# Kernel tuning notes

Hardware: AMD Instinct MI355X
Metric: run time of the kernel (lower is better)

## Reference

```python
import jax, jax.numpy as jnp
import numpy as np

B, T, H = 2, 1024, 4096
HK, HV, DK, DV = 8, 32, 64, 64
VPK = HV // HK            # value heads per key head = 4
KEY_DIM = HK * DK         # 512
VAL_DIM = HV * DV         # 2048
CONV_DIM = 2 * KEY_DIM + VAL_DIM  # 3072
KSZ = 4
EPS = 1e-5
L2_EPS = 1e-6


def _l2norm(x):
    return x * jax.lax.rsqrt(jnp.sum(x * x, axis=-1, keepdims=True) + L2_EPS)


def setup_inputs() -> dict:
    key = jax.random.key(0)
    ks = jax.random.split(key, 8)
    s = 0.02
    return {
        "hidden_states": jax.random.normal(ks[0], (B, T, H), jnp.float32),
        "W_qkvz": jax.random.normal(ks[1], (H, 2 * KEY_DIM + 2 * VAL_DIM), jnp.float32) * s,
        "W_ba": jax.random.normal(ks[2], (H, 2 * HV), jnp.float32) * s,
        "conv_w": jax.random.normal(ks[3], (CONV_DIM, KSZ), jnp.float32) * 0.1,
        "dt_bias": jnp.ones((HV,), jnp.float32),
        "A_log": jnp.log(jax.random.uniform(ks[4], (HV,), jnp.float32, 1.0, 16.0)),
        "norm_w": jnp.ones((DV,), jnp.float32),
        "W_out": jax.random.normal(ks[5], (VAL_DIM, H), jnp.float32) * s,
    }


def _forward(hidden_states, W_qkvz, W_ba, conv_w, dt_bias, A_log, norm_w, W_out):
    # --- projections ---
    qkvz = hidden_states @ W_qkvz                       # [B,T,5120]
    ba = hidden_states @ W_ba                           # [B,T,64]
    # fix_query_key_value_ordering: per key head [q(Dk), k(Dk), v(vpk*Dv), z(vpk*Dv)]
    qkvz = qkvz.reshape(B, T, HK, 2 * DK + 2 * VPK * DV)
    q = qkvz[..., :DK]                                  # [B,T,HK,DK]
    k = qkvz[..., DK:2 * DK]
    v = qkvz[..., 2 * DK:2 * DK + VPK * DV].reshape(B, T, HV, DV)
    z = qkvz[..., 2 * DK + VPK * DV:].reshape(B, T, HV, DV)
    ba = ba.reshape(B, T, HK, 2 * VPK)
    b = ba[..., :VPK].reshape(B, T, HV)
    a = ba[..., VPK:].reshape(B, T, HV)

    # --- causal depthwise conv over concatenated qkv, then silu ---
    mixed = jnp.concatenate(
        [q.reshape(B, T, KEY_DIM), k.reshape(B, T, KEY_DIM), v.reshape(B, T, VAL_DIM)], axis=-1)
    padded = jnp.pad(mixed, ((0, 0), (KSZ - 1, 0), (0, 0)))
    conv = sum(padded[:, j:j + T, :] * conv_w[:, j] for j in range(KSZ))
    conv = jax.nn.silu(conv)
    q = conv[..., :KEY_DIM].reshape(B, T, HK, DK)
    k = conv[..., KEY_DIM:2 * KEY_DIM].reshape(B, T, HK, DK)
    v = conv[..., 2 * KEY_DIM:].reshape(B, T, HV, DV)

    # --- fused GDN gating: g = -exp(A_log)*softplus(a+dt_bias), beta = sigmoid(b) ---
    g = -jnp.exp(A_log) * jax.nn.softplus(a + dt_bias)  # [B,T,HV]
    beta = jax.nn.sigmoid(b)                            # [B,T,HV]

    # --- q/k l2 norm + scale, broadcast key heads to value heads ---
    q = _l2norm(q) * (DK ** -0.5)
    k = _l2norm(k)
    q = jnp.repeat(q, VPK, axis=2)                      # [B,T,HV,DK]
    k = jnp.repeat(k, VPK, axis=2)

    # --- gated delta-rule recurrence over time ---
    def step(S, inp):
        qt, kt, vt, gt, bt = inp                        # qt/kt [B,HV,DK], vt [B,HV,DV]
        S = S * jnp.exp(gt)[..., None, None]            # decay
        pred = jnp.einsum('bhk,bhkv->bhv', kt, S)
        delta = (vt - pred) * bt[..., None]
        S = S + jnp.einsum('bhk,bhv->bhkv', kt, delta)
        o = jnp.einsum('bhk,bhkv->bhv', qt, S)
        return S, o

    xs = (q.transpose(1, 0, 2, 3), k.transpose(1, 0, 2, 3), v.transpose(1, 0, 2, 3),
          g.transpose(1, 0, 2), beta.transpose(1, 0, 2))
    S0 = jnp.zeros((B, HV, DK, DV), q.dtype)
    _, o = jax.lax.scan(step, S0, xs)                   # [T,B,HV,DV]
    o = o.transpose(1, 0, 2, 3)                         # [B,T,HV,DV]

    # --- gated RMSNorm (norm before gate) + out projection ---
    o_n = o * jax.lax.rsqrt(jnp.mean(o * o, axis=-1, keepdims=True) + EPS) * norm_w
    o_n = o_n * jax.nn.silu(z)
    return o_n.reshape(B, T, VAL_DIM) @ W_out           # [B,T,H]


def reference(hidden_states, W_qkvz, W_ba, conv_w, dt_bias, A_log, norm_w, W_out):
    return _forward(hidden_states, W_qkvz, W_ba, conv_w, dt_bias, A_log, norm_w, W_out)
```

## Files before the change

kernel.cpp:

```cpp
#include <hip/hip_runtime.h>
#include <hip/hip_bf16.h>
#include <cstdint>
#include <cstddef>


typedef __attribute__((ext_vector_type(8))) short short8;
typedef __attribute__((ext_vector_type(4))) float f32x4;

__device__ __forceinline__ short f2bf(float f) {
  union { float f; unsigned u; } x; x.f = f;
  unsigned r = x.u + 0x7fffu + ((x.u >> 16) & 1u);
  return (short)(r >> 16);
}

__device__ __forceinline__ void gl_lds16(const short* g, short* l) {
  __builtin_amdgcn_global_load_lds(
      (const __attribute__((address_space(1))) void*)g,
      (__attribute__((address_space(3))) void*)l, 16, 0, 0);
}

__global__ __launch_bounds__(256) void to_bf16_kernel(const float* __restrict__ x,
                                                      short* __restrict__ y) {
  int i = blockIdx.x * 256 + threadIdx.x;
  float4 v = ((const float4*)x)[i];
  ushort4 r;
  r.x = (unsigned short)f2bf(v.x);
  r.y = (unsigned short)f2bf(v.y);
  r.z = (unsigned short)f2bf(v.z);
  r.w = (unsigned short)f2bf(v.w);
  ((ushort4*)y)[i] = r;
}

__global__ __launch_bounds__(256) void transpose_w1(const float* __restrict__ Wq,
                                                    const float* __restrict__ Wba,
                                                    short* __restrict__ Wt) {
  __shared__ float tile[32][33];
  int n0 = blockIdx.x * 32;
  int k0 = blockIdx.y * 32;
  int t = threadIdx.x;
  int r = t >> 5;
  int c = t & 31;
#pragma unroll
  for (int i = 0; i < 4; ++i) {
    int kl = r + i * 8;
    int n = n0 + c;
    float v = 0.f;
    if (n < 5120) v = Wq[(size_t)(k0 + kl) * 5120 + n];
    else if (n < 5184) v = Wba[(size_t)(k0 + kl) * 64 + (n - 5120)];
    tile[kl][c] = v;
  }
  __syncthreads();
#pragma unroll
  for (int i = 0; i < 4; ++i) {
    int nl = r + i * 8;
    int kl = c;
    Wt[(size_t)(n0 + nl) * 4096 + k0 + kl] = f2bf(tile[kl][nl]);
  }
}

__global__ __launch_bounds__(256) void transpose_w2(const float* __restrict__ W,
                                                    short* __restrict__ Wt) {
  __shared__ float tile[32][33];
  int n0 = blockIdx.x * 32;
  int k0 = blockIdx.y * 32;
  int t = threadIdx.x;
  int r = t >> 5;
  int c = t & 31;
#pragma unroll
  for (int i = 0; i < 4; ++i) {
    int kl = r + i * 8;
    tile[kl][c] = W[(size_t)(k0 + kl) * 4096 + n0 + c];
  }
  __syncthreads();
#pragma unroll
  for (int i = 0; i < 4; ++i) {
    int nl = r + i * 8;
    int kl = c;
    Wt[(size_t)(n0 + nl) * 2048 + k0 + kl] = f2bf(tile[kl][nl]);
  }
}

template <bool GUARD_N>
__global__ __launch_bounds__(256) void gemm128(const short* __restrict__ A,
                                               const short* __restrict__ Bt,
                                               float* __restrict__ C,
                                               int M, int N, int K) {
  __shared__ __align__(16) short As[128 * 32];
  __shared__ __align__(16) short Bs[128 * 32];
  const int tid = threadIdx.x;
  const int wave = tid >> 6;
  const int lane = tid & 63;
  const int m0 = blockIdx.x * 128;
  const int n0 = blockIdx.y * 128;
  const int wm = (wave >> 1) << 6;
  const int wn = (wave & 1) << 6;

  const int srow = (wave << 4) + (lane >> 2);
  const int scol = (lane & 3) << 3;
  const short* Ag = A + (size_t)(m0 + srow) * K + scol;
  const short* Bg = Bt + (size_t)(n0 + srow) * K + scol;
  const size_t rstep = (size_t)64 * K;

  const int fr = lane & 15;
  const int kq = (lane >> 4) << 3;

  f32x4 acc[4][4];
#pragma unroll
  for (int i = 0; i < 4; ++i)
#pragma unroll
    for (int j = 0; j < 4; ++j) acc[i][j] = (f32x4){0.f, 0.f, 0.f, 0.f};

  for (int k0 = 0; k0 < K; k0 += 32) {
    __syncthreads();
    gl_lds16(Ag + k0,         &As[wave * 512]);
    gl_lds16(Ag + rstep + k0, &As[2048 + wave * 512]);
    gl_lds16(Bg + k0,         &Bs[wave * 512]);
    gl_lds16(Bg + rstep + k0, &Bs[2048 + wave * 512]);
    __syncthreads();
    short8 af[4], bf[4];
#pragma unroll
    for (int i = 0; i < 4; ++i) {
      af[i] = *(const short8*)&As[(wm + i * 16 + fr) * 32 + kq];
      bf[i] = *(const short8*)&Bs[(wn + i * 16 + fr) * 32 + kq];
    }
#pragma unroll
    for (int mt = 0; mt < 4; ++mt)
#pragma unroll
      for (int nt = 0; nt < 4; ++nt)
        acc[mt][nt] = __builtin_amdgcn_mfma_f32_16x16x32_bf16(af[mt], bf[nt], acc[mt][nt], 0, 0, 0);
  }

  const int rbase = (lane >> 4) << 2;
#pragma unroll
  for (int mt = 0; mt < 4; ++mt) {
#pragma unroll
    for (int nt = 0; nt < 4; ++nt) {
      int ncol = n0 + wn + nt * 16 + fr;
      if (GUARD_N && ncol >= N) continue;
      int mrow = m0 + wm + mt * 16 + rbase;
#pragma unroll
      for (int r = 0; r < 4; ++r)
        C[(size_t)(mrow + r) * N + ncol] = acc[mt][nt][r];
    }
  }
}

__global__ __launch_bounds__(256) void conv_kernel(const float* __restrict__ qkvz,
                                                   const float* __restrict__ conv_w,
                                                   float* __restrict__ mix) {
  __shared__ float sq[1024];
  __shared__ float scale[16];
  int bt = blockIdx.x;
  int t = bt & 1023;
  int tid = threadIdx.x;
  for (int c = tid; c < 3072; c += 256) {
    int col;
    if (c < 512) {
      col = (c >> 6) * 640 + (c & 63);
    } else if (c < 1024) {
      int c2 = c - 512;
      col = (c2 >> 6) * 640 + 64 + (c2 & 63);
    } else {
      int c3 = c - 1024;
      int hv = c3 >> 6;
      col = (hv >> 2) * 640 + 128 + (hv & 3) * 64 + (c3 & 63);
    }
    float acc = 0.f;
#pragma unroll
    for (int j = 0; j < 4; ++j) {
      int tt = t - 3 + j;
      if (tt >= 0) acc += qkvz[(size_t)(bt - 3 + j) * 5184 + col] * conv_w[c * 4 + j];
    }
    float sv = acc / (1.f + __expf(-acc));
    if (c < 1024)
      sq[c] = sv;
    else
      mix[(size_t)bt * 3072 + c] = sv;
  }
  __syncthreads();
  int g = tid >> 4, l = tid & 15;
  float p = 0.f;
#pragma unroll
  for (int i = 0; i < 4; ++i) {
    float v = sq[g * 64 + l * 4 + i];
    p += v * v;
  }
  p += __shfl_xor(p, 1);
  p += __shfl_xor(p, 2);
  p += __shfl_xor(p, 4);
  p += __shfl_xor(p, 8);
  if (l == 0) scale[g] = rsqrtf(p + 1e-6f);
  __syncthreads();
  for (int c = tid; c < 1024; c += 256) {
    float s = scale[c >> 6] * ((c < 512) ? 0.125f : 1.f);
    mix[(size_t)bt * 3072 + c] = sq[c] * s;
  }
}

__global__ __launch_bounds__(256) void gate_kernel(const float* __restrict__ qkvz,
                                                   const float* __restrict__ dt_bias,
                                                   const float* __restrict__ A_log,
                                                   float* __restrict__ gb,
                                                   float* __restrict__ beta) {
  int i = blockIdx.x * 256 + threadIdx.x;
  int hv = i & 31;
  int bt = i >> 5;
  int hk = hv >> 2, vp = hv & 3;
  const float* row = qkvz + (size_t)bt * 5184 + 5120 + hk * 8;
  float bv = row[vp];
  float av = row[4 + vp];
  float x = av + dt_bias[hv];
  float sp = (x > 20.f) ? x : log1pf(expf(x));
  gb[i] = -expf(A_log[hv]) * sp;
  beta[i] = 1.f / (1.f + expf(-bv));
}

__global__ __launch_bounds__(256) void precompute_kernel(
    const float* __restrict__ mix, const float* __restrict__ gbuf,
    const float* __restrict__ betab, float* __restrict__ Wbuf,
    float* __restrict__ Pbuf, float* __restrict__ Rbuf, float* __restrict__ cbuf) {
  __shared__ float Kt[64][68];
  __shared__ float Vb[64][68];
  __shared__ float AM[64][68];
  __shared__ float Mm[64][68];
  __shared__ float Tb[16][17];
  __shared__ float cs[64], bb[64];

  const int u = blockIdx.x;
  const int chunk = u & 15, hv = (u >> 4) & 31, b = u >> 9;
  const int hk = hv >> 2;
  const int t0g = b * 1024 + chunk * 64;
  const int tid = threadIdx.x;
  const int tr = tid >> 2, q4 = tid & 3;

  {
    const float* mrow = mix + (size_t)(t0g + tr) * 3072;
#pragma unroll
    for (int e = 0; e < 4; ++e) {
      int c0 = q4 * 16 + e * 4;
      float4 kv = *(const float4*)(mrow + 512 + hk * 64 + c0);
      Kt[c0 + 0][tr] = kv.x; Kt[c0 + 1][tr] = kv.y;
      Kt[c0 + 2][tr] = kv.z; Kt[c0 + 3][tr] = kv.w;
      *(float4*)&Vb[tr][c0] = *(const float4*)(mrow + 1024 + hv * 64 + c0);
    }
  }
  if (tid < 64) {
    cs[tid] = gbuf[(size_t)(t0g + tid) * 32 + hv];
    bb[tid] = betab[(size_t)(t0g + tid) * 32 + hv];
  }
  __syncthreads();
  for (int off = 1; off < 64; off <<= 1) {
    float v = 0.f;
    if (tid < 64 && tid >= off) v = cs[tid - off];
    __syncthreads();
    if (tid < 64) cs[tid] += v;
    __syncthreads();
  }
  if (tid < 64) cbuf[(size_t)u * 64 + tid] = cs[tid];

  {
    float acc[16];
#pragma unroll
    for (int i = 0; i < 16; ++i) acc[i] = 0.f;
    for (int d = 0; d < 64; ++d) {
      float kv = Kt[d][tr];
#pragma unroll
      for (int e = 0; e < 4; ++e) {
        float4 ks = *(const float4*)&Kt[d][q4 * 16 + e * 4];
        acc[e * 4 + 0] += kv * ks.x; acc[e * 4 + 1] += kv * ks.y;
        acc[e * 4 + 2] += kv * ks.z; acc[e * 4 + 3] += kv * ks.w;
      }
    }
    float bt_ = bb[tr], ct_ = cs[tr];
#pragma unroll
    for (int j = 0; j < 16; ++j) {
      int s = q4 * 16 + j;
      AM[tr][s] = (s < tr) ? bt_ * acc[j] * __expf(ct_ - cs[s]) : 0.f;
    }
  }
  __syncthreads();

  for (int i = tid; i < 64 * 68; i += 256) (&Mm[0][0])[i] = 0.f;
  __syncthreads();
  if (tid < 64) {
    int blk = tid >> 4, j = tid & 15, base = blk * 16;
    Mm[base][base + j] = (j == 0) ? 1.f : 0.f;
    for (int r = 1; r < 16; ++r) {
      float sum = 0.f;
      for (int s = 0; s < r; ++s) sum += AM[base + r][base + s] * Mm[base + s][base + j];
      Mm[base + r][base + j] = ((r == j) ? 1.f : 0.f) - sum;
    }
  }
  __syncthreads();
  for (int d = 1; d < 4; ++d) {
    for (int j = 0; j + d < 4; ++j) {
      int i = j + d;
      int r = tid >> 4, c = tid & 15;
      float tsum = 0.f;
      for (int kb = j; kb < i; ++kb)
        for (int uu = 0; uu < 16; ++uu)
          tsum += AM[i * 16 + r][kb * 16 + uu] * Mm[kb * 16 + uu][j * 16 + c];
      Tb[r][c] = tsum;
      __syncthreads();
      float msum = 0.f;
      for (int uu = 0; uu < 16; ++uu)
        msum += Mm[i * 16 + r][i * 16 + uu] * Tb[uu][c];
      __syncthreads();
      Mm[i * 16 + r][j * 16 + c] = -msum;
      __syncthreads();
    }
  }

  {
    const float* mrow = mix + (size_t)(t0g + tr) * 3072 + hk * 64;
#pragma unroll
    for (int e = 0; e < 4; ++e) {
      int c0 = q4 * 16 + e * 4;
      float4 qv = *(const float4*)(mrow + c0);
      AM[c0 + 0][tr] = qv.x; AM[c0 + 1][tr] = qv.y;
      AM[c0 + 2][tr] = qv.z; AM[c0 + 3][tr] = qv.w;
    }
  }
  __syncthreads();

  {
    float acc[16];
#pragma unroll
    for (int i = 0; i < 16; ++i) acc[i] = 0.f;
    for (int d = 0; d < 64; ++d) {
      float qv = AM[d][tr];
#pragma unroll
      for (int e = 0; e < 4; ++e) {
        float4 ks = *(const float4*)&Kt[d][q4 * 16 + e * 4];
        acc[e * 4 + 0] += qv * ks.x; acc[e * 4 + 1] += qv * ks.y;
        acc[e * 4 + 2] += qv * ks.z; acc[e * 4 + 3] += qv * ks.w;
      }
    }
    float ct_ = cs[tr];
#pragma unroll
    for (int e = 0; e < 4; ++e) {
      int s0 = q4 * 16 + e * 4;
      float4 pv;
      pv.x = (s0 + 0 <= tr) ? acc[e * 4 + 0] * __expf(ct_ - cs[s0 + 0]) : 0.f;
      pv.y = (s0 + 1 <= tr) ? acc[e * 4 + 1] * __expf(ct_ - cs[s0 + 1]) : 0.f;
      pv.z = (s0 + 2 <= tr) ? acc[e * 4 + 2] * __expf(ct_ - cs[s0 + 2]) : 0.f;
      pv.w = (s0 + 3 <= tr) ? acc[e * 4 + 3] * __expf(ct_ - cs[s0 + 3]) : 0.f;
      *(float4*)&Pbuf[(size_t)u * 4096 + tr * 64 + s0] = pv;
    }
  }
  __syncthreads();

  {
    float vals[16];
#pragma unroll
    for (int j = 0; j < 16; ++j) vals[j] = Kt[q4 * 16 + j][tr];
    float sc = bb[tr] * __expf(cs[tr]);
    __syncthreads();
#pragma unroll
    for (int j = 0; j < 16; ++j) Kt[tr][q4 * 16 + j] = vals[j] * sc;
  }
  __syncthreads();

  {
    float acc[16];
#pragma unroll
    for (int i = 0; i < 16; ++i) acc[i] = 0.f;
    for (int s = 0; s < 64; ++s) {
      float m = Mm[tr][s];
#pragma unroll
      for (int e = 0; e < 4; ++e) {
        float4 kk = *(const float4*)&Kt[s][q4 * 16 + e * 4];
        acc[e * 4 + 0] += m * kk.x; acc[e * 4 + 1] += m * kk.y;
        acc[e * 4 + 2] += m * kk.z; acc[e * 4 + 3] += m * kk.w;
      }
    }
#pragma unroll
    for (int e = 0; e < 4; ++e) {
      float4 wv = {acc[e * 4 + 0], acc[e * 4 + 1], acc[e * 4 + 2], acc[e * 4 + 3]};
      *(float4*)&Wbuf[(size_t)u * 4096 + tr * 64 + q4 * 16 + e * 4] = wv;
    }
  }
  {
    float acc[16];
#pragma unroll
    for (int i = 0; i < 16; ++i) acc[i] = 0.f;
    for (int s = 0; s < 64; ++s) {
      float m = Mm[tr][s] * bb[s];
#pragma unroll
      for (int e = 0; e < 4; ++e) {
        float4 vv = *(const float4*)&Vb[s][q4 * 16 + e * 4];
        acc[e * 4 + 0] += m * vv.x; acc[e * 4 + 1] += m * vv.y;
        acc[e * 4 + 2] += m * vv.z; acc[e * 4 + 3] += m * vv.w;
      }
    }
#pragma unroll
    for (int e = 0; e < 4; ++e) {
      float4 rv = {acc[e * 4 + 0], acc[e * 4 + 1], acc[e * 4 + 2], acc[e * 4 + 3]};
      *(float4*)&Rbuf[(size_t)u * 4096 + tr * 64 + q4 * 16 + e * 4] = rv;
    }
  }
}

__global__ __launch_bounds__(512) void chunk_scan_kernel(
    const float* __restrict__ mix, const float* __restrict__ Wbuf,
    const float* __restrict__ Pbuf, const float* __restrict__ Rbuf,
    const float* __restrict__ cbuf, float* __restrict__ o) {
  __shared__ float Wb[64][68], Pb[64][68], Qh[64][68], Kt[64][68];
  __shared__ float St[16][68], Dt[16][68];
  __shared__ float cs[64];

  const int bid = blockIdx.x;
  const int vs = bid & 3, hv = (bid >> 2) & 31, b = bid >> 7;
  const int hk = hv >> 2;
  const int bh = b * 32 + hv;
  const int ubase = bh * 16;
  const int tid = threadIdx.x;
  const int tr = tid >> 3, q8 = tid & 7;
  const int c0 = q8 * 2, c1 = q8 * 2 + 1;

  for (int i = tid; i < 16 * 68; i += 512) (&St[0][0])[i] = 0.f;

  float4 WN[2], PN[2], KN[2], QN[2];
  float2 RN;
  float cN = 0.f;
  float e63c = 1.f;

#define ISSUE_LOADS(c)                                                          \
  {                                                                             \
    size_t uu = (size_t)(ubase + (c));                                          \
    _Pragma("unroll") for (int i = 0; i < 2; ++i) {                             \
      WN[i] = ((const float4*)(Wbuf + uu * 4096))[tid + 512 * i];               \
      PN[i] = ((const float4*)(Pbuf + uu * 4096))[tid + 512 * i];               \
    }                                                                           \
    const float* mrow = mix + (size_t)(b * 1024 + (c) * 64 + tr) * 3072;        \
    _Pragma("unroll") for (int e = 0; e < 2; ++e) {                             \
      KN[e] = *(const float4*)(mrow + 512 + hk * 64 + q8 * 8 + e * 4);          \
      QN[e] = *(const float4*)(mrow + hk * 64 + q8 * 8 + e * 4);                \
    }                                                                           \
    RN = *(const float2*)(Rbuf + uu * 4096 + tr * 64 + vs * 16 + q8 * 2);       \
    if (tid < 64) cN = cbuf[uu * 64 + tid];                                     \
  }

#define COMMIT()                                                                \
  {                                                                             \
    _Pragma("unroll") for (int i = 0; i < 2; ++i) {                             \
      int flat = (tid + 512 * i) * 4;                                           \
      int rr = flat >> 6, cc = flat & 63;                                       \
      *(float4*)&Wb[rr][cc] = WN[i];                                            \
      *(float4*)&Pb[rr][cc] = PN[i];                                            \
    }                                                                           \
    if (tid < 64) cs[tid] = cN;                                                 \
    __syncthreads();                                                            \
    float csv = cs[tr], cs63 = cs[63];                                          \
    float sQv = __expf(csv), sKv = __expf(cs63 - csv);                          \
    e63c = __expf(cs63);                                                        \
    float4 qa, qb;                                                              \
    qa.x = QN[0].x * sQv; qa.y = QN[0].y * sQv;                                 \
    qa.z = QN[0].z * sQv; qa.w = QN[0].w * sQv;                                 \
    qb.x = QN[1].x * sQv; qb.y = QN[1].y * sQv;                                 \
    qb.z = QN[1].z * sQv; qb.w = QN[1].w * sQv;                                 \
    *(float4*)&Qh[tr][q8 * 8] = qa;                                             \
    *(float4*)&Qh[tr][q8 * 8 + 4] = qb;                                         \
    Kt[q8 * 8 + 0][tr] = KN[0].x * sKv;                                         \
    Kt[q8 * 8 + 1][tr] = KN[0].y * sKv;                                         \
    Kt[q8 * 8 + 2][tr] = KN[0].z * sKv;                                         \
    Kt[q8 * 8 + 3][tr] = KN[0].w * sKv;                                         \
    Kt[q8 * 8 + 4][tr] = KN[1].x * sKv;                                         \
    Kt[q8 * 8 + 5][tr] = KN[1].y * sKv;                                         \
    Kt[q8 * 8 + 6][tr] = KN[1].z * sKv;                                         \
    Kt[q8 * 8 + 7][tr] = KN[1].w * sKv;                                         \
  }

  ISSUE_LOADS(0);
  COMMIT();
  float2 Rv = RN;

  for (int c = 0; c < 16; ++c) {
    if (c < 15) ISSUE_LOADS(c + 1);
    float2 acc = Rv;
#pragma unroll 4
    for (int k = 0; k < 64; k += 4) {
      float4 w4 = *(const float4*)&Wb[tr][k];
      float4 sa = *(const float4*)&St[c0][k];
      float4 sb = *(const float4*)&St[c1][k];
      acc.x -= w4.x * sa.x + w4.y * sa.y + w4.z * sa.z + w4.w * sa.w;
      acc.y -= w4.x * sb.x + w4.y * sb.y + w4.z * sb.z + w4.w * sb.w;
    }
    Dt[c0][tr] = acc.x;
    Dt[c1][tr] = acc.y;
    __syncthreads();
    {
      float2 ao = {0.f, 0.f};
#pragma unroll 4
      for (int i = 0; i < 64; i += 4) {
        float4 p4 = *(const float4*)&Pb[tr][i];
        float4 q4 = *(const float4*)&Qh[tr][i];
        float4 da = *(const float4*)&Dt[c0][i];
        float4 db = *(const float4*)&Dt[c1][i];
        float4 sa = *(const float4*)&St[c0][i];
        float4 sb = *(const float4*)&St[c1][i];
        ao.x += p4.x * da.x + p4.y * da.y + p4.z * da.z + p4.w * da.w
              + q4.x * sa.x + q4.y * sa.y + q4.z * sa.z + q4.w * sa.w;
        ao.y += p4.x * db.x + p4.y * db.y + p4.z * db.z + p4.w * db.w
              + q4.x * sb.x + q4.y * sb.y + q4.z * sb.z + q4.w * sb.w;
      }
      *(float2*)&o[((size_t)(bh * 4 + vs) * 1024 + c * 64 + tr) * 16 + q8 * 2] = ao;
    }
    __syncthreads();
    {
      float sx = St[c0][tr] * e63c;
      float sy = St[c1][tr] * e63c;
#pragma unroll 4
      for (int t = 0; t < 64; t += 4) {
        float4 k4 = *(const float4*)&Kt[tr][t];
        float4 da = *(const float4*)&Dt[c0][t];
        float4 db = *(const float4*)&Dt[c1][t];
        sx += k4.x * da.x + k4.y * da.y + k4.z * da.z + k4.w * da.w;
        sy += k4.x * db.x + k4.y * db.y + k4.z * db.z + k4.w * db.w;
      }
      St[c0][tr] = sx;
      St[c1][tr] = sy;
    }
    if (c < 15) {
      COMMIT();
      Rv = RN;
    }
  }
#undef ISSUE_LOADS
#undef COMMIT
}

__global__ __launch_bounds__(256) void rms_gate_kernel(const float* __restrict__ o,
                                                       const float* __restrict__ qkvz,
                                                       const float* __restrict__ norm_w,
                                                       short* __restrict__ on) {
  int bid = blockIdx.x;
  int bh = bid >> 8;
  int tg = bid & 255;
  int b = bh >> 5, hv = bh & 31;
  int t = tg * 4 + (threadIdx.x >> 6);
  int d = threadIdx.x & 63;
  int bt = b * 1024 + t;
  int hk = hv >> 2, vp = hv & 3;
  float x = o[((size_t)(bh * 4 + (d >> 4)) * 1024 + t) * 16 + (d & 15)];
  float ss = x * x;
  ss += __shfl_xor(ss, 1);
  ss += __shfl_xor(ss, 2);
  ss += __shfl_xor(ss, 4);
  ss += __shfl_xor(ss, 8);
  ss += __shfl_xor(ss, 16);
  ss += __shfl_xor(ss, 32);
  float sc = rsqrtf(ss * (1.f / 64.f) + 1e-5f);
  float z = qkvz[(size_t)bt * 5184 + hk * 640 + 384 + vp * 64 + d];
  float val = x * sc * norm_w[d] * (z / (1.f + __expf(-z)));
  on[((size_t)bt * 32 + hv) * 64 + d] = f2bf(val);
}

extern "C" void kernel_launch(void* const* d_in, const int* in_sizes, int n_in,
                              void* d_out, int out_size, void* d_ws, size_t ws_size,
                              hipStream_t stream) {
  const float* hidden = (const float*)d_in[0];
  const float* W_qkvz = (const float*)d_in[1];
  const float* W_ba = (const float*)d_in[2];
  const float* conv_w = (const float*)d_in[3];
  const float* dt_bias = (const float*)d_in[4];
  const float* A_log = (const float*)d_in[5];
  const float* norm_w = (const float*)d_in[6];
  const float* W_out = (const float*)d_in[7];
  float* out = (float*)d_out;

  char* ws = (char*)d_ws;
  short* A_bf = (short*)(ws + 0);
  short* Wt1 = (short*)(ws + 16777216);
  short* Wt2 = (short*)(ws + 59768832);
  float* qkvz = (float*)(ws + 76546048);
  float* mix = (float*)(ws + 119013376);
  float* gbuf = (float*)(ws + 144179200);
  float* beta = (float*)(ws + 144441344);
  float* o = (float*)(ws + 144703488);
  short* on = (short*)(ws + 161480704);
  float* Wbuf = (float*)(ws + 169869312);
  float* Pbuf = (float*)(ws + 186646528);
  float* Rbuf = (float*)(ws + 203423744);
  float* cbuf = (float*)(ws + 220200960);

  to_bf16_kernel<<<8192, 256, 0, stream>>>(hidden, A_bf);
  transpose_w1<<<dim3(164, 128), 256, 0, stream>>>(W_qkvz, W_ba, Wt1);
  transpose_w2<<<dim3(128, 64), 256, 0, stream>>>(W_out, Wt2);
  gemm128<true><<<dim3(16, 41), 256, 0, stream>>>(A_bf, Wt1, qkvz, 2048, 5184, 4096);
  conv_kernel<<<2048, 256, 0, stream>>>(qkvz, conv_w, mix);
  gate_kernel<<<256, 256, 0, stream>>>(qkvz, dt_bias, A_log, gbuf, beta);
  precompute_kernel<<<1024, 256, 0, stream>>>(mix, gbuf, beta, Wbuf, Pbuf, Rbuf, cbuf);
  chunk_scan_kernel<<<256, 512, 0, stream>>>(mix, Wbuf, Pbuf, Rbuf, cbuf, o);
  rms_gate_kernel<<<16384, 256, 0, stream>>>(o, qkvz, norm_w, on);
  gemm128<false><<<dim3(16, 32), 256, 0, stream>>>(on, Wt2, out, 2048, 4096, 2048);
}
```

Before: 610.7 us.

## Use 256x256 triple-buffered swizzled MFMA GEMM for input projection

Adds a new gemm256 kernel with 256x256 output tiles, 512 threads, a three-stage LDS ring fed by direct global-to-LDS loads, an XOR-swizzled LDS layout, and split MFMA phases with priority hints. The input projection GEMM now uses it instead of the 128x128 kernel. The aim is more data reuse per tile and better hiding of load latency behind MFMA work. In exchange the grid shrinks to 168 blocks, which leaves many CUs idle. The last N tile also reads weight rows past the padded Wt1 region, though those results are masked on store.

```diff
diff --git a/kernel.cpp b/kernel.cpp
--- a/kernel.cpp
+++ b/kernel.cpp
@@ -77,6 +77,128 @@
     int nl = r + i * 8;
     int kl = c;
     Wt[(size_t)(n0 + nl) * 2048 + k0 + kl] = f2bf(tile[kl][nl]);
+  }
+}
+
+template <bool GUARD_N>
+__global__ __launch_bounds__(512) void gemm256(const short* __restrict__ A,
+                                               const short* __restrict__ Bt,
+                                               float* __restrict__ C,
+                                               int M, int N, int K) {
+  __shared__ __align__(16) short As[3 * 8192];
+  __shared__ __align__(16) short Bs[3 * 8192];
+  const int tid = threadIdx.x;
+  const int w = tid >> 6, lane = tid & 63;
+  const int wm = w >> 2, wn = w & 3;
+  const int m0 = blockIdx.x * 256, n0 = blockIdx.y * 256;
+  (void)M;
+
+  const int p0 = w * 64 + lane;
+  const int rp0 = p0 >> 3, q0 = p0 & 7;
+  const int mm0 = q0 ^ (rp0 & 7);
+  const int srow = rp0 * 2 + (mm0 >> 2);
+  const int scol = (mm0 & 3) << 3;
+  const short* Ag = A + (size_t)(m0 + srow) * K + scol;
+  const short* Bg = Bt + (size_t)(n0 + srow) * K + scol;
+  const size_t rstep = (size_t)128 * K;
+
+  const int fr = lane & 15;
+  const int s = lane >> 4;
+  int aoff[8], boff[4];
+#pragma unroll
+  for (int i = 0; i < 8; ++i) {
+    int row = wm * 128 + i * 16 + fr;
+    int rp = row >> 1;
+    int q = (((row & 1) << 2) | s) ^ (rp & 7);
+    aoff[i] = (rp * 8 + q) * 8;
+  }
+#pragma unroll
+  for (int j = 0; j < 4; ++j) {
+    int row = wn * 64 + j * 16 + fr;
+    int rp = row >> 1;
+    int q = (((row & 1) << 2) | s) ^ (rp & 7);
+    boff[j] = (rp * 8 + q) * 8;
+  }
+
+  f32x4 acc[8][4];
+#pragma unroll
+  for (int i = 0; i < 8; ++i)
+#pragma unroll
+    for (int j = 0; j < 4; ++j) acc[i][j] = (f32x4){0.f, 0.f, 0.f, 0.f};
+
+  const int NKT = K >> 5;
+
+#define STAGE_A(kt, bb)                                                \
+  { const short* g = Ag + (size_t)(kt) * 32;                           \
+    gl_lds16(g,         &As[(bb) * 8192 + w * 512]);                   \
+    gl_lds16(g + rstep, &As[(bb) * 8192 + 4096 + w * 512]); }
+#define STAGE_B(kt, bb)                                                \
+  { const short* g = Bg + (size_t)(kt) * 32;                           \
+    gl_lds16(g,         &Bs[(bb) * 8192 + w * 512]);                   \
+    gl_lds16(g + rstep, &Bs[(bb) * 8192 + 4096 + w * 512]); }
+
+  STAGE_A(0, 0); STAGE_B(0, 0);
+  STAGE_A(1, 1); STAGE_B(1, 1);
+  asm volatile("s_waitcnt vmcnt(4)" ::: "memory");
+  __builtin_amdgcn_s_barrier();
+  __builtin_amdgcn_sched_barrier(0);
+
+  int bi = 0;
+  for (int kt = 0; kt < NKT; ++kt) {
+    int bi2 = bi - 1; if (bi2 < 0) bi2 = 2;
+    const short* Ab = &As[bi * 8192];
+    const short* Bb = &Bs[bi * 8192];
+    short8 af[4], bf[4];
+#pragma unroll
+    for (int i = 0; i < 4; ++i) af[i] = *(const short8*)&Ab[aoff[i]];
+#pragma unroll
+    for (int j = 0; j < 4; ++j) bf[j] = *(const short8*)&Bb[boff[j]];
+    if (kt + 2 < NKT) STAGE_A(kt + 2, bi2);
+    __builtin_amdgcn_s_barrier();
+    asm volatile("s_waitcnt lgkmcnt(0)" ::: "memory");
+    __builtin_amdgcn_sched_barrier(0);
+    __builtin_amdgcn_s_setprio(1);
+#pragma unroll
+    for (int i = 0; i < 4; ++i)
+#pragma unroll
+      for (int j = 0; j < 4; ++j)
+        acc[i][j] = __builtin_amdgcn_mfma_f32_16x16x32_bf16(af[i], bf[j], acc[i][j], 0, 0, 0);
+    __builtin_amdgcn_s_setprio(0);
+    __builtin_amdgcn_sched_barrier(0);
+#pragma unroll
+    for (int i = 0; i < 4; ++i) af[i] = *(const short8*)&Ab[aoff[i + 4]];
+    if (kt + 2 < NKT) STAGE_B(kt + 2, bi2);
+    if (kt < NKT - 2) { asm volatile("s_waitcnt vmcnt(4)" ::: "memory"); }
+    else              { asm volatile("s_waitcnt vmcnt(0)" ::: "memory"); }
+    __builtin_amdgcn_s_barrier();
+    asm volatile("s_waitcnt lgkmcnt(0)" ::: "memory");
+    __builtin_amdgcn_sched_barrier(0);
+    __builtin_amdgcn_s_setprio(1);
+#pragma unroll
+    for (int i = 0; i < 4; ++i)
+#pragma unroll
+      for (int j = 0; j < 4; ++j)
+        acc[i + 4][j] = __builtin_amdgcn_mfma_f32_16x16x32_bf16(af[i], bf[j], acc[i + 4][j], 0, 0, 0);
+    __builtin_amdgcn_s_setprio(0);
+    __builtin_amdgcn_sched_barrier(0);
+    __builtin_amdgcn_s_barrier();
+    ++bi; if (bi == 3) bi = 0;
+  }
+#undef STAGE_A
+#undef STAGE_B
+
+  const int rbase = (lane >> 4) << 2;
+#pragma unroll
+  for (int i = 0; i < 8; ++i) {
+#pragma unroll
+    for (int j = 0; j < 4; ++j) {
+      int col = n0 + wn * 64 + j * 16 + fr;
+      if (GUARD_N && col >= N) continue;
+      int row = m0 + wm * 128 + i * 16 + rbase;
+#pragma unroll
+      for (int r = 0; r < 4; ++r)
+        C[(size_t)(row + r) * N + col] = acc[i][j][r];
+    }
   }
 }
 
@@ -587,7 +709,7 @@
   to_bf16_kernel<<<8192, 256, 0, stream>>>(hidden, A_bf);
   transpose_w1<<<dim3(164, 128), 256, 0, stream>>>(W_qkvz, W_ba, Wt1);
   transpose_w2<<<dim3(128, 64), 256, 0, stream>>>(W_out, Wt2);
-  gemm128<true><<<dim3(16, 41), 256, 0, stream>>>(A_bf, Wt1, qkvz, 2048, 5184, 4096);
+  gemm256<true><<<dim3(8, 21), 512, 0, stream>>>(A_bf, Wt1, qkvz, 2048, 5184, 4096);
   conv_kernel<<<2048, 256, 0, stream>>>(qkvz, conv_w, mix);
   gate_kernel<<<256, 256, 0, stream>>>(qkvz, dt_bias, A_log, gbuf, beta);
   precompute_kernel<<<1024, 256, 0, stream>>>(mix, gbuf, beta, Wbuf, Pbuf, Rbuf, cbuf);
```

Result: no change. 599.7 us (-1.8%).
